# Optimization experiments

Hardware: AMD Instinct MI355X
Metric: run time of the kernel (lower is better)

## Reference

```python
import jax, jax.numpy as jnp
import numpy as np

B, S, E, H = 512, 100, 256, 256
C_EXPLORE = 10.0  # tanh_exploration


def setup_inputs() -> dict:
    key = jax.random.key(0)
    ks = jax.random.split(key, 22)
    sH = 1.0 / np.sqrt(H)
    sE = 1.0 / np.sqrt(E)
    u = lambda k, shp, s: jax.random.uniform(k, shp, minval=-s, maxval=s, dtype=jnp.float32)
    return {
        "inputs": jax.random.uniform(ks[0], (B, 2, S), dtype=jnp.float32),  # 2D coords in [0,1)
        "emb": u(ks[1], (2, E), sE),
        "enc_Wih": u(ks[2], (4 * H, E), sH), "enc_Whh": u(ks[3], (4 * H, H), sH),
        "enc_bih": u(ks[4], (4 * H,), sH), "enc_bhh": u(ks[5], (4 * H,), sH),
        "dec_Wih": u(ks[6], (4 * H, E), sH), "dec_Whh": u(ks[7], (4 * H, H), sH),
        "dec_bih": u(ks[8], (4 * H,), sH), "dec_bhh": u(ks[9], (4 * H,), sH),
        "g_Wq": u(ks[10], (H, H), sH), "g_bq": u(ks[11], (H,), sH),
        "g_Wr": u(ks[12], (H, H), sH), "g_br": u(ks[13], (H,), sH),
        "g_V": u(ks[14], (H,), sH),
        "p_Wq": u(ks[15], (H, H), sH), "p_bq": u(ks[16], (H,), sH),
        "p_Wr": u(ks[17], (H, H), sH), "p_br": u(ks[18], (H,), sH),
        "p_V": u(ks[19], (H,), sH),
        "start": u(ks[20], (E,), sE),
    }


def _lstm_cell(x, h, c, Wih, Whh, bih, bhh):
    # torch LSTM gate order: input, forget, cell, output
    g = x @ Wih.T + h @ Whh.T + bih + bhh
    i, f, gg, o = jnp.split(g, 4, axis=-1)
    c = jax.nn.sigmoid(f) * c + jax.nn.sigmoid(i) * jnp.tanh(gg)
    return jax.nn.sigmoid(o) * jnp.tanh(c), c


def _forward(inputs, emb, enc_Wih, enc_Whh, enc_bih, enc_bhh,
             dec_Wih, dec_Whh, dec_bih, dec_bhh,
             g_Wq, g_bq, g_Wr, g_br, g_V,
             p_Wq, p_bq, p_Wr, p_br, p_V, start):
    # GraphEmbedding: per-position bmm([B,1,2],[B,2,E]) == single einsum
    embedded = jnp.einsum('bcs,ce->bse', inputs, emb)  # [B,S,E]

    h0 = jnp.zeros((B, H), jnp.float32)
    c0 = jnp.zeros((B, H), jnp.float32)

    def enc_step(carry, x_t):
        h, c = carry
        h, c = _lstm_cell(x_t, h, c, enc_Wih, enc_Whh, enc_bih, enc_bhh)
        return (h, c), h

    (h, c), outs = jax.lax.scan(enc_step, (h0, c0), embedded.transpose(1, 0, 2))
    enc = outs.transpose(1, 0, 2)  # encoder_outputs [B,S,H]

    # Conv1d(k=1) projection of encoder outputs is step-invariant: precompute once.
    ref_g = jnp.einsum('bsh,oh->bso', enc, g_Wr) + g_br  # [B,S,H]
    ref_p = jnp.einsum('bsh,oh->bso', enc, p_Wr) + p_br  # [B,S,H]

    keys = jax.random.split(jax.random.key(1), S)
    arange_b = jnp.arange(B)

    def attn(q, ref_proj, Wq, bq, V):
        qq = q @ Wq.T + bq  # [B,H]
        return jnp.einsum('h,bsh->bs', V, jnp.tanh(qq[:, None, :] + ref_proj))

    def step(carry, k):
        h, c, mask, idxs, valid, dec_in = carry
        h, c = _lstm_cell(dec_in, h, c, dec_Wih, dec_Whh, dec_bih, dec_bhh)
        # apply_mask_to_logits: mask grows by idxs only after first selection
        mask = jnp.where(valid, mask.at[arange_b, idxs].set(True), mask)
        # glimpse (n_glimpses = 1, use_tanh=False)
        lg = jnp.where(mask, -jnp.inf, attn(h, ref_g, g_Wq, g_bq, g_V))
        q = jnp.einsum('bsh,bs->bh', enc, jax.nn.softmax(lg, axis=-1))
        # pointer (use_tanh=True, C=10)
        lp = C_EXPLORE * jnp.tanh(attn(q, ref_p, p_Wq, p_bq, p_V))
        lp = jnp.where(mask, -jnp.inf, lp)
        probs = jax.nn.softmax(lp, axis=-1)
        idxs = jax.random.categorical(k, lp)  # multinomial(probs, 1)
        dec_in = embedded[arange_b, idxs]
        return (h, c, mask, idxs, jnp.array(True), dec_in), (probs, idxs)

    init = (h, c, jnp.zeros((B, S), bool), jnp.zeros((B,), jnp.int32),
            jnp.array(False), jnp.broadcast_to(start, (B, E)))
    _, (probs, idxs) = jax.lax.scan(step, init, keys)
    return probs, idxs  # [S,B,S] float, [S,B] int


def reference(inputs, emb, enc_Wih, enc_Whh, enc_bih, enc_bhh,
              dec_Wih, dec_Whh, dec_bih, dec_bhh,
              g_Wq, g_bq, g_Wr, g_br, g_V,
              p_Wq, p_bq, p_Wr, p_br, p_V, start):
    return _forward(inputs, emb, enc_Wih, enc_Whh, enc_bih, enc_bhh,
                    dec_Wih, dec_Whh, dec_bih, dec_bhh,
                    g_Wq, g_bq, g_Wr, g_br, g_V,
                    p_Wq, p_bq, p_Wr, p_br, p_V, start)
```

## Files before the change

kernel.cpp:

```cpp
#include <hip/hip_runtime.h>
#include <cstdint>
#include <math.h>

#define B_ 512
#define S_ 100
#define E_ 256
#define H_ 256

__device__ __forceinline__ float sigmoidf_(float x){ return 1.0f/(1.0f+expf(-x)); }

__device__ __forceinline__ void threefry2x32_(uint32_t k0, uint32_t k1,
                                              uint32_t c0, uint32_t c1,
                                              uint32_t& o0, uint32_t& o1){
  uint32_t ks2 = k0 ^ k1 ^ 0x1BD11BDAu;
  uint32_t x0 = c0 + k0, x1 = c1 + k1;
#define ROT_(x,d) (((x)<<(d))|((x)>>(32-(d))))
#define RND_(r) { x0 += x1; x1 = ROT_(x1,(r)); x1 ^= x0; }
  RND_(13) RND_(15) RND_(26) RND_(6)  x0 += k1;  x1 += ks2 + 1u;
  RND_(17) RND_(29) RND_(16) RND_(24) x0 += ks2; x1 += k0  + 2u;
  RND_(13) RND_(15) RND_(26) RND_(6)  x0 += k0;  x1 += k1  + 3u;
  RND_(17) RND_(29) RND_(16) RND_(24) x0 += k1;  x1 += ks2 + 4u;
  RND_(13) RND_(15) RND_(26) RND_(6)  x0 += ks2; x1 += k0  + 5u;
#undef RND_
#undef ROT_
  o0 = x0; o1 = x1;
}

__device__ __forceinline__ float gumbel_bits_(uint32_t bits){
  const float tiny = 1.175494350822287508e-38f;
  float u = __uint_as_float((bits >> 9) | 0x3f800000u) - 1.0f;
  u = fmaxf(tiny, u + tiny);
  return -logf(-logf(u));
}

__device__ __forceinline__ float wsum_(float v){
  #pragma unroll
  for (int d = 32; d > 0; d >>= 1) v += __shfl_xor(v, d, 64);
  return v;
}
__device__ __forceinline__ float wmax_(float v){
  #pragma unroll
  for (int d = 32; d > 0; d >>= 1) v = fmaxf(v, __shfl_xor(v, d, 64));
  return v;
}

__global__ __launch_bounds__(256) void prep_w4(const float* __restrict__ Wih,
                                               const float* __restrict__ Whh,
                                               float* __restrict__ W4){
  int idx = blockIdx.x*256 + threadIdx.x;
  int g = idx & 3, u = (idx >> 2) & 255, k = idx >> 10;
  int row = g*256 + u;
  W4[idx] = (k < 256) ? Wih[row*256 + k] : Whh[row*256 + (k-256)];
}
__global__ __launch_bounds__(256) void prep_b4(const float* __restrict__ b1,
                                               const float* __restrict__ b2,
                                               float* __restrict__ o){
  int idx = blockIdx.x*256 + threadIdx.x;
  if (idx < 1024) {
    int g = idx & 3, u = idx >> 2;
    o[idx] = b1[g*256 + u] + b2[g*256 + u];
  }
}
__global__ __launch_bounds__(256) void transpose256(const float* __restrict__ src,
                                                    float* __restrict__ dst){
  int idx = blockIdx.x*256 + threadIdx.x;
  int r = idx >> 8, cc = idx & 255;
  dst[idx] = src[cc*256 + r];
}
__global__ __launch_bounds__(256) void init_state(float* __restrict__ h, float* __restrict__ c,
                                                  int* __restrict__ mask, int* __restrict__ sel){
  int i = blockIdx.x*256 + threadIdx.x;
  if (i < B_*H_) { h[i] = 0.f; c[i] = 0.f; }
  if (i < B_*S_) mask[i] = 0;
  if (i < B_)    sel[i]  = -1;
}

__global__ __launch_bounds__(256) void lstm_step2(
    const float* __restrict__ W4,
    const float* __restrict__ b4,
    const float* __restrict__ coords,
    const float* __restrict__ emb,
    const float* __restrict__ start,
    const int*   __restrict__ sel,
    const float* __restrict__ hr,
    float* __restrict__ hw,
    float* __restrict__ cst,
    float* __restrict__ enc_out,
    int t, int mode)
{
  const int tid = threadIdx.x;
  const int uu  = tid & 63;
  const int rg  = tid >> 6;
  const int b0  = (blockIdx.x >> 2) * 8;
  const int u0  = (blockIdx.x & 3) * 64;
  __shared__ float Xs[512*8];

  for (int i = tid; i < 4096; i += 256) {
    const int k = i >> 3, r = i & 7, b = b0 + r;
    float v;
    if (k < 256) {
      if (mode == 0) {
        v = coords[b*200 + t]*emb[k] + coords[b*200 + 100 + t]*emb[256 + k];
      } else {
        const int s = sel[b];
        if (s < 0) v = start[k];
        else       v = coords[b*200 + s]*emb[k] + coords[b*200 + 100 + s]*emb[256 + k];
      }
    } else {
      v = hr[b*256 + (k - 256)];
    }
    Xs[i] = v;
  }
  __syncthreads();

  float a0x=0.f,a0y=0.f,a0z=0.f,a0w=0.f, a1x=0.f,a1y=0.f,a1z=0.f,a1w=0.f;
  const float* wp = W4 + (size_t)(u0 + uu)*4;
  #pragma unroll 4
  for (int k = 0; k < 512; ++k) {
    const float4 w = *(const float4*)(wp + (size_t)k*1024);
    const float2 x = *(const float2*)(Xs + k*8 + rg*2);
    a0x += x.x*w.x; a0y += x.x*w.y; a0z += x.x*w.z; a0w += x.x*w.w;
    a1x += x.y*w.x; a1y += x.y*w.y; a1z += x.y*w.z; a1w += x.y*w.w;
  }

  const float4 bb = *(const float4*)(b4 + (u0 + uu)*4);
  const int u = u0 + uu;
  {
    const int b = b0 + rg*2;
    const float gi = a0x + bb.x, gf = a0y + bb.y, gg = a0z + bb.z, go = a0w + bb.w;
    const float cN = sigmoidf_(gf)*cst[b*256+u] + sigmoidf_(gi)*tanhf(gg);
    const float hN = sigmoidf_(go)*tanhf(cN);
    cst[b*256+u] = cN; hw[b*256+u] = hN;
    if (mode == 0) enc_out[((size_t)b*S_ + t)*H_ + u] = hN;
  }
  {
    const int b = b0 + rg*2 + 1;
    const float gi = a1x + bb.x, gf = a1y + bb.y, gg = a1z + bb.z, go = a1w + bb.w;
    const float cN = sigmoidf_(gf)*cst[b*256+u] + sigmoidf_(gi)*tanhf(gg);
    const float hN = sigmoidf_(go)*tanhf(cN);
    cst[b*256+u] = cN; hw[b*256+u] = hN;
    if (mode == 0) enc_out[((size_t)b*S_ + t)*H_ + u] = hN;
  }
}

__global__ __launch_bounds__(256) void matvec_bias(
    const float* __restrict__ X, const float* __restrict__ WT,
    const float* __restrict__ bias, float* __restrict__ out)
{
  const int tid = threadIdx.x;
  const int b0 = blockIdx.x * 4;
  __shared__ float Xs[1024];
  for (int i = tid; i < 1024; i += 256)
    Xs[i] = X[(b0 + (i & 3))*256 + (i >> 2)];
  __syncthreads();
  float a0 = bias[tid];
  float a1 = a0, a2 = a0, a3 = a0;
  #pragma unroll 4
  for (int k = 0; k < 256; ++k) {
    const float w = WT[k*256 + tid];
    const float4 x = *(const float4*)(Xs + k*4);
    a0 += x.x*w; a1 += x.y*w; a2 += x.z*w; a3 += x.w*w;
  }
  out[(b0+0)*256 + tid] = a0;
  out[(b0+1)*256 + tid] = a1;
  out[(b0+2)*256 + tid] = a2;
  out[(b0+3)*256 + tid] = a3;
}

__global__ __launch_bounds__(256) void glimpse_step(
    const float* __restrict__ qqIn, const float* __restrict__ enc,
    const float* __restrict__ ref_g, const float* __restrict__ g_V,
    const int* __restrict__ mask, float* __restrict__ qOut)
{
  const int b = blockIdx.x, tid = threadIdx.x, lane = tid & 63, wv = tid >> 6;
  __shared__ float qqs[256], gVs[256], lg[128], alpha[128];
  qqs[tid] = qqIn[b*256 + tid];
  gVs[tid] = g_V[tid];
  __syncthreads();

  const float* rg = ref_g + (size_t)b*S_*H_;
  const int* mk = mask + b*S_;
  for (int is = 0; is < 25; ++is) {
    const int s = is*4 + wv;
    float p = 0.f;
    #pragma unroll
    for (int j = 0; j < 4; ++j) {
      const int hh = lane + 64*j;
      p += gVs[hh] * tanhf(qqs[hh] + rg[s*256 + hh]);
    }
    p = wsum_(p);
    if (lane == 0) lg[s] = mk[s] ? -INFINITY : p;
  }
  __syncthreads();

  if (wv == 0) {
    const float v0 = lg[lane];
    const float v1 = (lane + 64 < S_) ? lg[lane + 64] : -INFINITY;
    const float m  = wmax_(fmaxf(v0, v1));
    const float e0 = expf(v0 - m);
    const float e1 = (lane + 64 < S_) ? expf(v1 - m) : 0.f;
    const float sm = wsum_(e0 + e1);
    alpha[lane] = e0 / sm;
    if (lane + 64 < S_) alpha[lane + 64] = e1 / sm;
  }
  __syncthreads();

  const float* eb = enc + (size_t)b*S_*H_;
  float a = 0.f;
  for (int s = 0; s < S_; ++s) a += alpha[s] * eb[s*256 + tid];
  qOut[b*256 + tid] = a;
}

__global__ __launch_bounds__(256) void pointer_step(
    const float* __restrict__ pqIn, const float* __restrict__ ref_p,
    const float* __restrict__ p_V,
    int* __restrict__ mask, int* __restrict__ sel,
    float* __restrict__ probs_out, float* __restrict__ idx_out, int t)
{
  const int b = blockIdx.x, tid = threadIdx.x, lane = tid & 63, wv = tid >> 6;
  __shared__ float pqs[256], pVs[256], lp[128];
  pqs[tid] = pqIn[b*256 + tid];
  pVs[tid] = p_V[tid];
  __syncthreads();

  const float* rp = ref_p + (size_t)b*S_*H_;
  const int* mk = mask + b*S_;
  for (int is = 0; is < 25; ++is) {
    const int s = is*4 + wv;
    float p = 0.f;
    #pragma unroll
    for (int j = 0; j < 4; ++j) {
      const int hh = lane + 64*j;
      p += pVs[hh] * tanhf(pqs[hh] + rp[s*256 + hh]);
    }
    p = wsum_(p);
    if (lane == 0) {
      const float v = 10.0f * tanhf(p);
      lp[s] = mk[s] ? -INFINITY : v;
    }
  }
  __syncthreads();

  if (wv == 0) {
    const float v0 = lp[lane];
    const float v1 = (lane + 64 < S_) ? lp[lane + 64] : -INFINITY;
    const float m  = wmax_(fmaxf(v0, v1));
    const float e0 = expf(v0 - m);
    const float e1 = (lane + 64 < S_) ? expf(v1 - m) : 0.f;
    const float sm = wsum_(e0 + e1);
    float* po = probs_out + ((size_t)t*B_ + b)*S_;
    po[lane] = e0 / sm;
    if (lane + 64 < S_) po[lane + 64] = e1 / sm;

    uint32_t k0, k1; threefry2x32_(0u, 1u, 0u, (uint32_t)t, k0, k1);
    uint32_t r0, r1;
    threefry2x32_(k0, k1, 0u, (uint32_t)(b*S_ + lane), r0, r1);
    float z0 = v0 + gumbel_bits_(r0 ^ r1);
    float z1 = -INFINITY;
    if (lane + 64 < S_) {
      uint32_t q0, q1;
      threefry2x32_(k0, k1, 0u, (uint32_t)(b*S_ + lane + 64), q0, q1);
      z1 = v1 + gumbel_bits_(q0 ^ q1);
    }
    float bv; int bi;
    if (z1 > z0) { bv = z1; bi = lane + 64; } else { bv = z0; bi = lane; }
    #pragma unroll
    for (int d = 32; d > 0; d >>= 1) {
      const float ov = __shfl_xor(bv, d, 64);
      const int   oi = __shfl_xor(bi, d, 64);
      if (ov > bv || (ov == bv && oi < bi)) { bv = ov; bi = oi; }
    }
    if (lane == 0) {
      idx_out[t*B_ + b] = (float)bi;
      sel[b] = bi;
      mask[b*S_ + bi] = 1;
    }
  }
}

__global__ __launch_bounds__(256) void gemm_ref(
    const float* __restrict__ A, const float* __restrict__ Bt,
    const float* __restrict__ bias, float* __restrict__ C)
{
  const int tid = threadIdx.x;
  const int m0 = blockIdx.x * 128, n0 = blockIdx.y * 128;
  __shared__ float As[8][128];
  __shared__ float Bs[8][128];
  float acc[8][8] = {};
  const int tx = tid & 15, ty = tid >> 4;

  for (int k0 = 0; k0 < 256; k0 += 8) {
    {
      const int row = tid >> 1, q = tid & 1;
      const float4 av = *(const float4*)(A + (size_t)(m0+row)*256 + k0 + q*4);
      As[q*4+0][row] = av.x; As[q*4+1][row] = av.y;
      As[q*4+2][row] = av.z; As[q*4+3][row] = av.w;
    }
    {
      const int kk = tid >> 5, nq = tid & 31;
      *(float4*)(&Bs[kk][nq*4]) = *(const float4*)(Bt + (size_t)(k0+kk)*256 + n0 + nq*4);
    }
    __syncthreads();
    #pragma unroll
    for (int k = 0; k < 8; ++k) {
      float a[8], bb[8];
      *(float4*)&a[0]  = *(const float4*)&As[k][ty*8];
      *(float4*)&a[4]  = *(const float4*)&As[k][ty*8+4];
      *(float4*)&bb[0] = *(const float4*)&Bs[k][tx*8];
      *(float4*)&bb[4] = *(const float4*)&Bs[k][tx*8+4];
      #pragma unroll
      for (int i = 0; i < 8; ++i)
        #pragma unroll
        for (int j = 0; j < 8; ++j)
          acc[i][j] += a[i]*bb[j];
    }
    __syncthreads();
  }
  #pragma unroll
  for (int i = 0; i < 8; ++i) {
    const int m = m0 + ty*8 + i;
    #pragma unroll
    for (int j = 0; j < 8; j += 4) {
      const int n = n0 + tx*8 + j;
      float4 o;
      o.x = acc[i][j  ] + bias[n  ];
      o.y = acc[i][j+1] + bias[n+1];
      o.z = acc[i][j+2] + bias[n+2];
      o.w = acc[i][j+3] + bias[n+3];
      *(float4*)(C + (size_t)m*256 + n) = o;
    }
  }
}

extern "C" void kernel_launch(void* const* d_in, const int* in_sizes, int n_in,
                              void* d_out, int out_size, void* d_ws, size_t ws_size,
                              hipStream_t stream) {
  (void)in_sizes; (void)n_in; (void)out_size; (void)ws_size;
  const float* inputs = (const float*)d_in[0];
  const float* emb    = (const float*)d_in[1];
  const float* eWih   = (const float*)d_in[2];
  const float* eWhh   = (const float*)d_in[3];
  const float* ebih   = (const float*)d_in[4];
  const float* ebhh   = (const float*)d_in[5];
  const float* dWih   = (const float*)d_in[6];
  const float* dWhh   = (const float*)d_in[7];
  const float* dbih   = (const float*)d_in[8];
  const float* dbhh   = (const float*)d_in[9];
  const float* gWq    = (const float*)d_in[10];
  const float* gbq    = (const float*)d_in[11];
  const float* gWr    = (const float*)d_in[12];
  const float* gbr    = (const float*)d_in[13];
  const float* gV     = (const float*)d_in[14];
  const float* pWq    = (const float*)d_in[15];
  const float* pbq    = (const float*)d_in[16];
  const float* pWr    = (const float*)d_in[17];
  const float* pbr    = (const float*)d_in[18];
  const float* pV     = (const float*)d_in[19];
  const float* start  = (const float*)d_in[20];

  float* ws = (float*)d_ws;
  size_t o = 0;
  float* W4E  = ws + o; o += (size_t)512*1024;
  float* W4D  = ws + o; o += (size_t)512*1024;
  float* b4E  = ws + o; o += 1024;
  float* b4D  = ws + o; o += 1024;
  float* gWqT = ws + o; o += 65536;
  float* pWqT = ws + o; o += 65536;
  float* gWrT = ws + o; o += 65536;
  float* pWrT = ws + o; o += 65536;
  float* enc  = ws + o; o += (size_t)B_*S_*H_;
  float* refg = ws + o; o += (size_t)B_*S_*H_;
  float* refp = ws + o; o += (size_t)B_*S_*H_;
  float* h0   = ws + o; o += (size_t)B_*H_;
  float* h1   = ws + o; o += (size_t)B_*H_;
  float* c    = ws + o; o += (size_t)B_*H_;
  float* qq   = ws + o; o += (size_t)B_*H_;
  float* qb   = ws + o; o += (size_t)B_*H_;
  float* pq   = ws + o; o += (size_t)B_*H_;
  int* mask   = (int*)(ws + o); o += (size_t)B_*S_;
  int* sel    = (int*)(ws + o); o += B_;

  float* probs = (float*)d_out;
  float* idxo  = probs + (size_t)S_*B_*S_;

  float* hpp[2] = {h0, h1};
  int p = 0;

  prep_w4<<<2048,256,0,stream>>>(eWih, eWhh, W4E);
  prep_w4<<<2048,256,0,stream>>>(dWih, dWhh, W4D);
  prep_b4<<<4,256,0,stream>>>(ebih, ebhh, b4E);
  prep_b4<<<4,256,0,stream>>>(dbih, dbhh, b4D);
  transpose256<<<256,256,0,stream>>>(gWq, gWqT);
  transpose256<<<256,256,0,stream>>>(pWq, pWqT);
  transpose256<<<256,256,0,stream>>>(gWr, gWrT);
  transpose256<<<256,256,0,stream>>>(pWr, pWrT);
  init_state<<<512,256,0,stream>>>(h0, c, mask, sel);

  for (int t = 0; t < S_; ++t) {
    lstm_step2<<<256,256,0,stream>>>(W4E, b4E, inputs, emb, nullptr, nullptr,
                                     hpp[p], hpp[1-p], c, enc, t, 0);
    p ^= 1;
  }

  gemm_ref<<<dim3(400,2),256,0,stream>>>(enc, gWrT, gbr, refg);
  gemm_ref<<<dim3(400,2),256,0,stream>>>(enc, pWrT, pbr, refp);

  for (int t = 0; t < S_; ++t) {
    lstm_step2<<<256,256,0,stream>>>(W4D, b4D, inputs, emb, start, sel,
                                     hpp[p], hpp[1-p], c, nullptr, t, 1);
    p ^= 1;
    matvec_bias<<<128,256,0,stream>>>(hpp[p], gWqT, gbq, qq);
    glimpse_step<<<512,256,0,stream>>>(qq, enc, refg, gV, mask, qb);
    matvec_bias<<<128,256,0,stream>>>(qb, pWqT, pbq, pq);
    pointer_step<<<512,256,0,stream>>>(pq, refp, pV, mask, sel, probs, idxo, t);
  }
}
```

Baseline: 22.27 ms.

## Fuse whole pointer network into one persistent cooperative kernel with grid syncs

Result: slower. 42.45 ms (+90.6%).

```diff
diff --git a/kernel.cpp b/kernel.cpp
--- a/kernel.cpp
+++ b/kernel.cpp
@@ -1,6 +1,9 @@
 #include <hip/hip_runtime.h>
+#include <hip/hip_cooperative_groups.h>
 #include <cstdint>
 #include <math.h>
+
+namespace cg = cooperative_groups;
 
 #define B_ 512
 #define S_ 100
@@ -44,72 +47,54 @@
   return v;
 }
 
-__global__ __launch_bounds__(256) void prep_w4(const float* __restrict__ Wih,
-                                               const float* __restrict__ Whh,
-                                               float* __restrict__ W4){
-  int idx = blockIdx.x*256 + threadIdx.x;
-  int g = idx & 3, u = (idx >> 2) & 255, k = idx >> 10;
-  int row = g*256 + u;
-  W4[idx] = (k < 256) ? Wih[row*256 + k] : Whh[row*256 + (k-256)];
-}
-__global__ __launch_bounds__(256) void prep_b4(const float* __restrict__ b1,
-                                               const float* __restrict__ b2,
-                                               float* __restrict__ o){
-  int idx = blockIdx.x*256 + threadIdx.x;
-  if (idx < 1024) {
-    int g = idx & 3, u = idx >> 2;
-    o[idx] = b1[g*256 + u] + b2[g*256 + u];
-  }
-}
-__global__ __launch_bounds__(256) void transpose256(const float* __restrict__ src,
-                                                    float* __restrict__ dst){
-  int idx = blockIdx.x*256 + threadIdx.x;
-  int r = idx >> 8, cc = idx & 255;
-  dst[idx] = src[cc*256 + r];
-}
-__global__ __launch_bounds__(256) void init_state(float* __restrict__ h, float* __restrict__ c,
-                                                  int* __restrict__ mask, int* __restrict__ sel){
-  int i = blockIdx.x*256 + threadIdx.x;
-  if (i < B_*H_) { h[i] = 0.f; c[i] = 0.f; }
-  if (i < B_*S_) mask[i] = 0;
-  if (i < B_)    sel[i]  = -1;
-}
-
-__global__ __launch_bounds__(256) void lstm_step2(
-    const float* __restrict__ W4,
-    const float* __restrict__ b4,
-    const float* __restrict__ coords,
-    const float* __restrict__ emb,
-    const float* __restrict__ start,
-    const int*   __restrict__ sel,
-    const float* __restrict__ hr,
-    float* __restrict__ hw,
-    float* __restrict__ cst,
-    float* __restrict__ enc_out,
-    int t, int mode)
+struct KParams {
+  const float *inputs, *emb;
+  const float *eWih, *eWhh, *ebih, *ebhh;
+  const float *dWih, *dWhh, *dbih, *dbhh;
+  const float *gWq, *gbq, *gWr, *gbr, *gV;
+  const float *pWq, *pbq, *pWr, *pbr, *pV;
+  const float *start;
+  float *W4E, *W4D, *b4E, *b4D, *gWqT, *pWqT, *gWrT, *pWrT;
+  float *enc, *refg, *refp, *h0, *h1, *c;
+  float *probs, *idxo;
+  int *mask, *sel;
+};
+
+union SMem {
+  float xs[4096];
+  struct { float As[8][128]; float Bs[8][128]; } g;
+  struct {
+    float qq[2][256]; float q[2][256]; float pq[2][256];
+    float lg[128]; float alpha[2][128]; float lp[128];
+  } a;
+};
+
+__device__ void lstm_phase(const KParams& P, SMem& sm,
+                           const float* __restrict__ W4, const float* __restrict__ b4,
+                           const float* __restrict__ hr, float* __restrict__ hw,
+                           float* __restrict__ cst, float* enc_out, int t, int mode)
 {
   const int tid = threadIdx.x;
   const int uu  = tid & 63;
   const int rg  = tid >> 6;
   const int b0  = (blockIdx.x >> 2) * 8;
   const int u0  = (blockIdx.x & 3) * 64;
-  __shared__ float Xs[512*8];
 
   for (int i = tid; i < 4096; i += 256) {
     const int k = i >> 3, r = i & 7, b = b0 + r;
     float v;
     if (k < 256) {
       if (mode == 0) {
-        v = coords[b*200 + t]*emb[k] + coords[b*200 + 100 + t]*emb[256 + k];
+        v = P.inputs[b*200 + t]*P.emb[k] + P.inputs[b*200 + 100 + t]*P.emb[256 + k];
       } else {
-        const int s = sel[b];
-        if (s < 0) v = start[k];
-        else       v = coords[b*200 + s]*emb[k] + coords[b*200 + 100 + s]*emb[256 + k];
+        const int s = P.sel[b];
+        if (s < 0) v = P.start[k];
+        else       v = P.inputs[b*200 + s]*P.emb[k] + P.inputs[b*200 + 100 + s]*P.emb[256 + k];
       }
     } else {
       v = hr[b*256 + (k - 256)];
     }
-    Xs[i] = v;
+    sm.xs[i] = v;
   }
   __syncthreads();
 
@@ -118,7 +103,7 @@
   #pragma unroll 4
   for (int k = 0; k < 512; ++k) {
     const float4 w = *(const float4*)(wp + (size_t)k*1024);
-    const float2 x = *(const float2*)(Xs + k*8 + rg*2);
+    const float2 x = *(const float2*)(sm.xs + k*8 + rg*2);
     a0x += x.x*w.x; a0y += x.x*w.y; a0z += x.x*w.z; a0w += x.x*w.w;
     a1x += x.y*w.x; a1y += x.y*w.y; a1z += x.y*w.z; a1w += x.y*w.w;
   }
@@ -141,151 +126,141 @@
     cst[b*256+u] = cN; hw[b*256+u] = hN;
     if (mode == 0) enc_out[((size_t)b*S_ + t)*H_ + u] = hN;
   }
-}
-
-__global__ __launch_bounds__(256) void matvec_bias(
-    const float* __restrict__ X, const float* __restrict__ WT,
-    const float* __restrict__ bias, float* __restrict__ out)
+  __syncthreads();
+}
+
+__device__ void attn_phase(const KParams& P, SMem& sm, const float* __restrict__ h, int t)
+{
+  const int tid = threadIdx.x, lane = tid & 63, wv = tid >> 6;
+  const int b0 = blockIdx.x * 2;
+
+  {
+    float a0 = P.gbq[tid], a1 = a0;
+    const float* h0r = h + (size_t)b0*256;
+    const float* h1r = h + (size_t)(b0+1)*256;
+    #pragma unroll 4
+    for (int k = 0; k < 256; ++k) {
+      const float w = P.gWqT[k*256 + tid];
+      a0 += h0r[k]*w; a1 += h1r[k]*w;
+    }
+    sm.a.qq[0][tid] = a0; sm.a.qq[1][tid] = a1;
+  }
+  __syncthreads();
+
+  for (int bb = 0; bb < 2; ++bb) {
+    const float* rg = P.refg + (size_t)(b0+bb)*S_*H_;
+    const int* mk = P.mask + (b0+bb)*S_;
+    for (int is = 0; is < 25; ++is) {
+      const int s = is*4 + wv;
+      float pp = 0.f;
+      #pragma unroll
+      for (int j = 0; j < 4; ++j) {
+        const int hh = lane + 64*j;
+        pp += P.gV[hh] * tanhf(sm.a.qq[bb][hh] + rg[s*256 + hh]);
+      }
+      pp = wsum_(pp);
+      if (lane == 0) sm.a.lg[s] = mk[s] ? -INFINITY : pp;
+    }
+    __syncthreads();
+    if (wv == 0) {
+      const float v0 = sm.a.lg[lane];
+      const float v1 = (lane + 64 < S_) ? sm.a.lg[lane + 64] : -INFINITY;
+      const float m  = wmax_(fmaxf(v0, v1));
+      const float e0 = expf(v0 - m);
+      const float e1 = (lane + 64 < S_) ? expf(v1 - m) : 0.f;
+      const float smm = wsum_(e0 + e1);
+      sm.a.alpha[bb][lane] = e0 / smm;
+      if (lane + 64 < S_) sm.a.alpha[bb][lane + 64] = e1 / smm;
+    }
+    __syncthreads();
+  }
+
+  {
+    const float* e0p = P.enc + (size_t)b0*S_*H_;
+    const float* e1p = P.enc + (size_t)(b0+1)*S_*H_;
+    float a0 = 0.f, a1 = 0.f;
+    for (int s = 0; s < S_; ++s) {
+      a0 += sm.a.alpha[0][s] * e0p[s*256 + tid];
+      a1 += sm.a.alpha[1][s] * e1p[s*256 + tid];
+    }
+    sm.a.q[0][tid] = a0; sm.a.q[1][tid] = a1;
+  }
+  __syncthreads();
+
+  {
+    float a0 = P.pbq[tid], a1 = a0;
+    #pragma unroll 4
+    for (int k = 0; k < 256; ++k) {
+      const float w = P.pWqT[k*256 + tid];
+      a0 += sm.a.q[0][k]*w; a1 += sm.a.q[1][k]*w;
+    }
+    sm.a.pq[0][tid] = a0; sm.a.pq[1][tid] = a1;
+  }
+  __syncthreads();
+
+  for (int bb = 0; bb < 2; ++bb) {
+    const int b = b0 + bb;
+    const float* rp = P.refp + (size_t)b*S_*H_;
+    const int* mk = P.mask + b*S_;
+    for (int is = 0; is < 25; ++is) {
+      const int s = is*4 + wv;
+      float pp = 0.f;
+      #pragma unroll
+      for (int j = 0; j < 4; ++j) {
+        const int hh = lane + 64*j;
+        pp += P.pV[hh] * tanhf(sm.a.pq[bb][hh] + rp[s*256 + hh]);
+      }
+      pp = wsum_(pp);
+      if (lane == 0) {
+        const float v = 10.0f * tanhf(pp);
+        sm.a.lp[s] = mk[s] ? -INFINITY : v;
+      }
+    }
+    __syncthreads();
+    if (wv == 0) {
+      const float v0 = sm.a.lp[lane];
+      const float v1 = (lane + 64 < S_) ? sm.a.lp[lane + 64] : -INFINITY;
+      const float m  = wmax_(fmaxf(v0, v1));
+      const float e0 = expf(v0 - m);
+      const float e1 = (lane + 64 < S_) ? expf(v1 - m) : 0.f;
+      const float smm = wsum_(e0 + e1);
+      float* po = P.probs + ((size_t)t*B_ + b)*S_;
+      po[lane] = e0 / smm;
+      if (lane + 64 < S_) po[lane + 64] = e1 / smm;
+
+      uint32_t k0, k1; threefry2x32_(0u, 1u, 0u, (uint32_t)t, k0, k1);
+      uint32_t r0, r1;
+      threefry2x32_(k0, k1, 0u, (uint32_t)(b*S_ + lane), r0, r1);
+      float z0 = v0 + gumbel_bits_(r0 ^ r1);
+      float z1 = -INFINITY;
+      if (lane + 64 < S_) {
+        uint32_t q0, q1;
+        threefry2x32_(k0, k1, 0u, (uint32_t)(b*S_ + lane + 64), q0, q1);
+        z1 = v1 + gumbel_bits_(q0 ^ q1);
+      }
+      float bv; int bi;
+      if (z1 > z0) { bv = z1; bi = lane + 64; } else { bv = z0; bi = lane; }
+      #pragma unroll
+      for (int d = 32; d > 0; d >>= 1) {
+        const float ov = __shfl_xor(bv, d, 64);
+        const int   oi = __shfl_xor(bi, d, 64);
+        if (ov > bv || (ov == bv && oi < bi)) { bv = ov; bi = oi; }
+      }
+      if (lane == 0) {
+        P.idxo[t*B_ + b] = (float)bi;
+        P.sel[b] = bi;
+        P.mask[b*S_ + bi] = 1;
+      }
+    }
+    __syncthreads();
+  }
+}
+
+__device__ void gemm_tile(SMem& sm, const float* __restrict__ A, const float* __restrict__ Bt,
+                          const float* __restrict__ bias, float* __restrict__ C,
+                          int m0, int n0)
 {
   const int tid = threadIdx.x;
-  const int b0 = blockIdx.x * 4;
-  __shared__ float Xs[1024];
-  for (int i = tid; i < 1024; i += 256)
-    Xs[i] = X[(b0 + (i & 3))*256 + (i >> 2)];
-  __syncthreads();
-  float a0 = bias[tid];
-  float a1 = a0, a2 = a0, a3 = a0;
-  #pragma unroll 4
-  for (int k = 0; k < 256; ++k) {
-    const float w = WT[k*256 + tid];
-    const float4 x = *(const float4*)(Xs + k*4);
-    a0 += x.x*w; a1 += x.y*w; a2 += x.z*w; a3 += x.w*w;
-  }
-  out[(b0+0)*256 + tid] = a0;
-  out[(b0+1)*256 + tid] = a1;
-  out[(b0+2)*256 + tid] = a2;
-  out[(b0+3)*256 + tid] = a3;
-}
-
-__global__ __launch_bounds__(256) void glimpse_step(
-    const float* __restrict__ qqIn, const float* __restrict__ enc,
-    const float* __restrict__ ref_g, const float* __restrict__ g_V,
-    const int* __restrict__ mask, float* __restrict__ qOut)
-{
-  const int b = blockIdx.x, tid = threadIdx.x, lane = tid & 63, wv = tid >> 6;
-  __shared__ float qqs[256], gVs[256], lg[128], alpha[128];
-  qqs[tid] = qqIn[b*256 + tid];
-  gVs[tid] = g_V[tid];
-  __syncthreads();
-
-  const float* rg = ref_g + (size_t)b*S_*H_;
-  const int* mk = mask + b*S_;
-  for (int is = 0; is < 25; ++is) {
-    const int s = is*4 + wv;
-    float p = 0.f;
-    #pragma unroll
-    for (int j = 0; j < 4; ++j) {
-      const int hh = lane + 64*j;
-      p += gVs[hh] * tanhf(qqs[hh] + rg[s*256 + hh]);
-    }
-    p = wsum_(p);
-    if (lane == 0) lg[s] = mk[s] ? -INFINITY : p;
-  }
-  __syncthreads();
-
-  if (wv == 0) {
-    const float v0 = lg[lane];
-    const float v1 = (lane + 64 < S_) ? lg[lane + 64] : -INFINITY;
-    const float m  = wmax_(fmaxf(v0, v1));
-    const float e0 = expf(v0 - m);
-    const float e1 = (lane + 64 < S_) ? expf(v1 - m) : 0.f;
-    const float sm = wsum_(e0 + e1);
-    alpha[lane] = e0 / sm;
-    if (lane + 64 < S_) alpha[lane + 64] = e1 / sm;
-  }
-  __syncthreads();
-
-  const float* eb = enc + (size_t)b*S_*H_;
-  float a = 0.f;
-  for (int s = 0; s < S_; ++s) a += alpha[s] * eb[s*256 + tid];
-  qOut[b*256 + tid] = a;
-}
-
-__global__ __launch_bounds__(256) void pointer_step(
-    const float* __restrict__ pqIn, const float* __restrict__ ref_p,
-    const float* __restrict__ p_V,
-    int* __restrict__ mask, int* __restrict__ sel,
-    float* __restrict__ probs_out, float* __restrict__ idx_out, int t)
-{
-  const int b = blockIdx.x, tid = threadIdx.x, lane = tid & 63, wv = tid >> 6;
-  __shared__ float pqs[256], pVs[256], lp[128];
-  pqs[tid] = pqIn[b*256 + tid];
-  pVs[tid] = p_V[tid];
-  __syncthreads();
-
-  const float* rp = ref_p + (size_t)b*S_*H_;
-  const int* mk = mask + b*S_;
-  for (int is = 0; is < 25; ++is) {
-    const int s = is*4 + wv;
-    float p = 0.f;
-    #pragma unroll
-    for (int j = 0; j < 4; ++j) {
-      const int hh = lane + 64*j;
-      p += pVs[hh] * tanhf(pqs[hh] + rp[s*256 + hh]);
-    }
-    p = wsum_(p);
-    if (lane == 0) {
-      const float v = 10.0f * tanhf(p);
-      lp[s] = mk[s] ? -INFINITY : v;
-    }
-  }
-  __syncthreads();
-
-  if (wv == 0) {
-    const float v0 = lp[lane];
-    const float v1 = (lane + 64 < S_) ? lp[lane + 64] : -INFINITY;
-    const float m  = wmax_(fmaxf(v0, v1));
-    const float e0 = expf(v0 - m);
-    const float e1 = (lane + 64 < S_) ? expf(v1 - m) : 0.f;
-    const float sm = wsum_(e0 + e1);
-    float* po = probs_out + ((size_t)t*B_ + b)*S_;
-    po[lane] = e0 / sm;
-    if (lane + 64 < S_) po[lane + 64] = e1 / sm;
-
-    uint32_t k0, k1; threefry2x32_(0u, 1u, 0u, (uint32_t)t, k0, k1);
-    uint32_t r0, r1;
-    threefry2x32_(k0, k1, 0u, (uint32_t)(b*S_ + lane), r0, r1);
-    float z0 = v0 + gumbel_bits_(r0 ^ r1);
-    float z1 = -INFINITY;
-    if (lane + 64 < S_) {
-      uint32_t q0, q1;
-      threefry2x32_(k0, k1, 0u, (uint32_t)(b*S_ + lane + 64), q0, q1);
-      z1 = v1 + gumbel_bits_(q0 ^ q1);
-    }
-    float bv; int bi;
-    if (z1 > z0) { bv = z1; bi = lane + 64; } else { bv = z0; bi = lane; }
-    #pragma unroll
-    for (int d = 32; d > 0; d >>= 1) {
-      const float ov = __shfl_xor(bv, d, 64);
-      const int   oi = __shfl_xor(bi, d, 64);
-      if (ov > bv || (ov == bv && oi < bi)) { bv = ov; bi = oi; }
-    }
-    if (lane == 0) {
-      idx_out[t*B_ + b] = (float)bi;
-      sel[b] = bi;
-      mask[b*S_ + bi] = 1;
-    }
-  }
-}
-
-__global__ __launch_bounds__(256) void gemm_ref(
-    const float* __restrict__ A, const float* __restrict__ Bt,
-    const float* __restrict__ bias, float* __restrict__ C)
-{
-  const int tid = threadIdx.x;
-  const int m0 = blockIdx.x * 128, n0 = blockIdx.y * 128;
-  __shared__ float As[8][128];
-  __shared__ float Bs[8][128];
   float acc[8][8] = {};
   const int tx = tid & 15, ty = tid >> 4;
 
@@ -293,21 +268,21 @@
     {
       const int row = tid >> 1, q = tid & 1;
       const float4 av = *(const float4*)(A + (size_t)(m0+row)*256 + k0 + q*4);
-      As[q*4+0][row] = av.x; As[q*4+1][row] = av.y;
-      As[q*4+2][row] = av.z; As[q*4+3][row] = av.w;
+      sm.g.As[q*4+0][row] = av.x; sm.g.As[q*4+1][row] = av.y;
+      sm.g.As[q*4+2][row] = av.z; sm.g.As[q*4+3][row] = av.w;
     }
     {
       const int kk = tid >> 5, nq = tid & 31;
-      *(float4*)(&Bs[kk][nq*4]) = *(const float4*)(Bt + (size_t)(k0+kk)*256 + n0 + nq*4);
+      *(float4*)(&sm.g.Bs[kk][nq*4]) = *(const float4*)(Bt + (size_t)(k0+kk)*256 + n0 + nq*4);
     }
     __syncthreads();
     #pragma unroll
     for (int k = 0; k < 8; ++k) {
       float a[8], bb[8];
-      *(float4*)&a[0]  = *(const float4*)&As[k][ty*8];
-      *(float4*)&a[4]  = *(const float4*)&As[k][ty*8+4];
-      *(float4*)&bb[0] = *(const float4*)&Bs[k][tx*8];
-      *(float4*)&bb[4] = *(const float4*)&Bs[k][tx*8+4];
+      *(float4*)&a[0]  = *(const float4*)&sm.g.As[k][ty*8];
+      *(float4*)&a[4]  = *(const float4*)&sm.g.As[k][ty*8+4];
+      *(float4*)&bb[0] = *(const float4*)&sm.g.Bs[k][tx*8];
+      *(float4*)&bb[4] = *(const float4*)&sm.g.Bs[k][tx*8+4];
       #pragma unroll
       for (int i = 0; i < 8; ++i)
         #pragma unroll
@@ -330,33 +305,70 @@
       *(float4*)(C + (size_t)m*256 + n) = o;
     }
   }
+  __syncthreads();
+}
+
+__global__ __launch_bounds__(256) void pointer_net_mono(KParams P)
+{
+  cg::grid_group gg = cg::this_grid();
+  __shared__ SMem sm;
+  const int tid = threadIdx.x;
+  const int gtid = blockIdx.x*256 + tid;
+
+  for (int i = gtid; i < 512*1024; i += 65536) {
+    const int g = i & 3, u = (i >> 2) & 255, k = i >> 10;
+    const int row = g*256 + u;
+    P.W4E[i] = (k < 256) ? P.eWih[row*256 + k] : P.eWhh[row*256 + (k-256)];
+    P.W4D[i] = (k < 256) ? P.dWih[row*256 + k] : P.dWhh[row*256 + (k-256)];
+  }
+  if (gtid < 1024) {
+    const int g = gtid & 3, u = gtid >> 2;
+    P.b4E[gtid] = P.ebih[g*256 + u] + P.ebhh[g*256 + u];
+    P.b4D[gtid] = P.dbih[g*256 + u] + P.dbhh[g*256 + u];
+  }
+  {
+    const int r = gtid >> 8, cc = gtid & 255;
+    P.gWqT[gtid] = P.gWq[cc*256 + r];
+    P.pWqT[gtid] = P.pWq[cc*256 + r];
+    P.gWrT[gtid] = P.gWr[cc*256 + r];
+    P.pWrT[gtid] = P.pWr[cc*256 + r];
+  }
+  for (int i = gtid; i < B_*H_; i += 65536) { P.h0[i] = 0.f; P.c[i] = 0.f; }
+  if (gtid < B_*S_) P.mask[gtid] = 0;
+  if (gtid < B_)    P.sel[gtid]  = -1;
+  __threadfence(); gg.sync();
+
+  float* hp[2] = { P.h0, P.h1 };
+  int p = 0;
+
+  for (int t = 0; t < S_; ++t) {
+    lstm_phase(P, sm, P.W4E, P.b4E, hp[p], hp[p^1], P.c, P.enc, t, 0);
+    p ^= 1;
+    __threadfence(); gg.sync();
+  }
+
+  for (int job = blockIdx.x; job < 1600; job += 256) {
+    const float* Bt   = (job < 800) ? P.gWrT : P.pWrT;
+    const float* bias = (job < 800) ? P.gbr  : P.pbr;
+    float* C          = (job < 800) ? P.refg : P.refp;
+    const int jj = job % 800;
+    gemm_tile(sm, P.enc, Bt, bias, C, (jj % 400)*128, (jj / 400)*128);
+  }
+  __threadfence(); gg.sync();
+
+  for (int t = 0; t < S_; ++t) {
+    lstm_phase(P, sm, P.W4D, P.b4D, hp[p], hp[p^1], P.c, nullptr, t, 1);
+    p ^= 1;
+    __threadfence(); gg.sync();
+    attn_phase(P, sm, hp[p], t);
+    __threadfence(); gg.sync();
+  }
 }
 
 extern "C" void kernel_launch(void* const* d_in, const int* in_sizes, int n_in,
                               void* d_out, int out_size, void* d_ws, size_t ws_size,
                               hipStream_t stream) {
   (void)in_sizes; (void)n_in; (void)out_size; (void)ws_size;
-  const float* inputs = (const float*)d_in[0];
-  const float* emb    = (const float*)d_in[1];
-  const float* eWih   = (const float*)d_in[2];
-  const float* eWhh   = (const float*)d_in[3];
-  const float* ebih   = (const float*)d_in[4];
-  const float* ebhh   = (const float*)d_in[5];
-  const float* dWih   = (const float*)d_in[6];
-  const float* dWhh   = (const float*)d_in[7];
-  const float* dbih   = (const float*)d_in[8];
-  const float* dbhh   = (const float*)d_in[9];
-  const float* gWq    = (const float*)d_in[10];
-  const float* gbq    = (const float*)d_in[11];
-  const float* gWr    = (const float*)d_in[12];
-  const float* gbr    = (const float*)d_in[13];
-  const float* gV     = (const float*)d_in[14];
-  const float* pWq    = (const float*)d_in[15];
-  const float* pbq    = (const float*)d_in[16];
-  const float* pWr    = (const float*)d_in[17];
-  const float* pbr    = (const float*)d_in[18];
-  const float* pV     = (const float*)d_in[19];
-  const float* start  = (const float*)d_in[20];
 
   float* ws = (float*)d_ws;
   size_t o = 0;
@@ -374,44 +386,40 @@
   float* h0   = ws + o; o += (size_t)B_*H_;
   float* h1   = ws + o; o += (size_t)B_*H_;
   float* c    = ws + o; o += (size_t)B_*H_;
-  float* qq   = ws + o; o += (size_t)B_*H_;
-  float* qb   = ws + o; o += (size_t)B_*H_;
-  float* pq   = ws + o; o += (size_t)B_*H_;
   int* mask   = (int*)(ws + o); o += (size_t)B_*S_;
   int* sel    = (int*)(ws + o); o += B_;
 
-  float* probs = (float*)d_out;
-  float* idxo  = probs + (size_t)S_*B_*S_;
-
-  float* hpp[2] = {h0, h1};
-  int p = 0;
-
-  prep_w4<<<2048,256,0,stream>>>(eWih, eWhh, W4E);
-  prep_w4<<<2048,256,0,stream>>>(dWih, dWhh, W4D);
-  prep_b4<<<4,256,0,stream>>>(ebih, ebhh, b4E);
-  prep_b4<<<4,256,0,stream>>>(dbih, dbhh, b4D);
-  transpose256<<<256,256,0,stream>>>(gWq, gWqT);
-  transpose256<<<256,256,0,stream>>>(pWq, pWqT);
-  transpose256<<<256,256,0,stream>>>(gWr, gWrT);
-  transpose256<<<256,256,0,stream>>>(pWr, pWrT);
-  init_state<<<512,256,0,stream>>>(h0, c, mask, sel);
-
-  for (int t = 0; t < S_; ++t) {
-    lstm_step2<<<256,256,0,stream>>>(W4E, b4E, inputs, emb, nullptr, nullptr,
-                                     hpp[p], hpp[1-p], c, enc, t, 0);
-    p ^= 1;
-  }
-
-  gemm_ref<<<dim3(400,2),256,0,stream>>>(enc, gWrT, gbr, refg);
-  gemm_ref<<<dim3(400,2),256,0,stream>>>(enc, pWrT, pbr, refp);
-
-  for (int t = 0; t < S_; ++t) {
-    lstm_step2<<<256,256,0,stream>>>(W4D, b4D, inputs, emb, start, sel,
-                                     hpp[p], hpp[1-p], c, nullptr, t, 1);
-    p ^= 1;
-    matvec_bias<<<128,256,0,stream>>>(hpp[p], gWqT, gbq, qq);
-    glimpse_step<<<512,256,0,stream>>>(qq, enc, refg, gV, mask, qb);
-    matvec_bias<<<128,256,0,stream>>>(qb, pWqT, pbq, pq);
-    pointer_step<<<512,256,0,stream>>>(pq, refp, pV, mask, sel, probs, idxo, t);
-  }
-}
+  KParams P;
+  P.inputs = (const float*)d_in[0];
+  P.emb    = (const float*)d_in[1];
+  P.eWih   = (const float*)d_in[2];
+  P.eWhh   = (const float*)d_in[3];
+  P.ebih   = (const float*)d_in[4];
+  P.ebhh   = (const float*)d_in[5];
+  P.dWih   = (const float*)d_in[6];
+  P.dWhh   = (const float*)d_in[7];
+  P.dbih   = (const float*)d_in[8];
+  P.dbhh   = (const float*)d_in[9];
+  P.gWq    = (const float*)d_in[10];
+  P.gbq    = (const float*)d_in[11];
+  P.gWr    = (const float*)d_in[12];
+  P.gbr    = (const float*)d_in[13];
+  P.gV     = (const float*)d_in[14];
+  P.pWq    = (const float*)d_in[15];
+  P.pbq    = (const float*)d_in[16];
+  P.pWr    = (const float*)d_in[17];
+  P.pbr    = (const float*)d_in[18];
+  P.pV     = (const float*)d_in[19];
+  P.start  = (const float*)d_in[20];
+  P.W4E = W4E; P.W4D = W4D; P.b4E = b4E; P.b4D = b4D;
+  P.gWqT = gWqT; P.pWqT = pWqT; P.gWrT = gWrT; P.pWrT = pWrT;
+  P.enc = enc; P.refg = refg; P.refp = refp;
+  P.h0 = h0; P.h1 = h1; P.c = c;
+  P.probs = (float*)d_out;
+  P.idxo  = P.probs + (size_t)S_*B_*S_;
+  P.mask = mask; P.sel = sel;
+
+  void* kargs[] = { (void*)&P };
+  hipLaunchCooperativeKernel((const void*)pointer_net_mono, dim3(256), dim3(256),
+                             kargs, 0, stream);
+}
```
